# Performance work log

Hardware: AMD Instinct MI355X
Metric: run time of the kernel (lower is better)

## Reference

```python
import jax, jax.numpy as jnp
import numpy as np

# Model dims (mamba_ssm defaults: expand=2, d_state=16, d_conv=4, dt_rank=ceil(d_model/16))
V, D_MODEL, N_LAYERS = 32000, 768, 2
D_INNER, D_STATE, D_CONV, DT_RANK = 1536, 16, 4, 48
BATCH, SEQ = 2, 2048


def setup_inputs() -> dict:
    key = jax.random.key(0)
    ks = jax.random.split(key, 10)

    def nrm(k, shape, s=0.02):
        return (jax.random.normal(k, shape) * s).astype(jnp.float32)

    x = jax.random.randint(ks[0], (BATCH, SEQ), 0, V)
    emb = nrm(ks[1], (V, D_MODEL))
    # per-layer Mamba params, stacked on leading layer axis
    W_in = nrm(ks[2], (N_LAYERS, 2 * D_INNER, D_MODEL))          # in_proj (no bias)
    conv_w = nrm(ks[3], (N_LAYERS, D_INNER, 1, D_CONV), 0.1)      # depthwise causal conv
    conv_b = jnp.zeros((N_LAYERS, D_INNER), jnp.float32)
    W_x = nrm(ks[4], (N_LAYERS, DT_RANK + 2 * D_STATE, D_INNER))  # x_proj (no bias)
    W_dt = nrm(ks[5], (N_LAYERS, D_INNER, DT_RANK), 0.05)         # dt_proj
    b_dt = jnp.full((N_LAYERS, D_INNER), -4.0, jnp.float32)       # softplus(-4) ~ small dt
    # A initialized as -exp(A_log) with A_log = log(1..d_state), per mamba_ssm
    A_log = jnp.log(jnp.broadcast_to(
        jnp.arange(1, D_STATE + 1, dtype=jnp.float32), (N_LAYERS, D_INNER, D_STATE)))
    D_skip = jnp.ones((N_LAYERS, D_INNER), jnp.float32)
    W_out = nrm(ks[6], (N_LAYERS, D_MODEL, D_INNER))              # out_proj (no bias)
    ln_g = jnp.ones((D_MODEL,), jnp.float32)
    ln_b = jnp.zeros((D_MODEL,), jnp.float32)
    head_w = nrm(ks[7], (V, D_MODEL))
    head_b = jnp.zeros((V,), jnp.float32)
    return dict(x=x, emb=emb, W_in=W_in, conv_w=conv_w, conv_b=conv_b, W_x=W_x,
                W_dt=W_dt, b_dt=b_dt, A_log=A_log, D_skip=D_skip, W_out=W_out,
                ln_g=ln_g, ln_b=ln_b, head_w=head_w, head_b=head_b)


def mamba_block(h, W_in, conv_w, conv_b, W_x, W_dt, b_dt, A_log, D_skip, W_out):
    # h: (B, L, D_MODEL)
    xz = jnp.einsum('bld,ed->ble', h, W_in)              # (B, L, 2*d_inner)
    u, z = jnp.split(xz, 2, axis=-1)
    # causal depthwise conv over time
    uc = jnp.transpose(u, (0, 2, 1))                     # (B, d_inner, L)
    uc = jax.lax.conv_general_dilated(
        uc, conv_w, window_strides=(1,), padding=[(D_CONV - 1, 0)],
        feature_group_count=D_INNER, dimension_numbers=('NCH', 'OIH', 'NCH'))
    u = jax.nn.silu(jnp.transpose(uc, (0, 2, 1)) + conv_b)
    # input-dependent dt, B, C
    x_dbl = jnp.einsum('bld,ed->ble', u, W_x)            # (B, L, dt_rank+2*d_state)
    dtl, Bm, Cm = jnp.split(x_dbl, [DT_RANK, DT_RANK + D_STATE], axis=-1)
    dt = jax.nn.softplus(jnp.einsum('blr,dr->bld', dtl, W_dt) + b_dt)  # (B, L, d_inner)
    A = -jnp.exp(A_log)                                  # (d_inner, d_state)

    def step(hst, inp):
        dt_t, u_t, B_t, C_t = inp                        # (B,d_inner),(B,d_inner),(B,d_state),(B,d_state)
        hst = jnp.exp(dt_t[..., None] * A) * hst + (dt_t * u_t)[..., None] * B_t[:, None, :]
        y_t = jnp.einsum('bds,bs->bd', hst, C_t)
        return hst, y_t

    h0 = jnp.zeros((u.shape[0], D_INNER, D_STATE), u.dtype)
    xs = (dt.transpose(1, 0, 2), u.transpose(1, 0, 2),
          Bm.transpose(1, 0, 2), Cm.transpose(1, 0, 2))
    _, ys = jax.lax.scan(step, h0, xs)                   # (L, B, d_inner)
    y = ys.transpose(1, 0, 2) + u * D_skip
    y = y * jax.nn.silu(z)
    return jnp.einsum('bli,oi->blo', y, W_out)           # back to (B, L, D_MODEL)


def reference(x, emb, W_in, conv_w, conv_b, W_x, W_dt, b_dt, A_log, D_skip,
              W_out, ln_g, ln_b, head_w, head_b):
    h = emb[x]                                           # (B, L, D_MODEL)
    for l in range(N_LAYERS):
        h = h + mamba_block(h, W_in[l], conv_w[l], conv_b[l], W_x[l], W_dt[l],
                            b_dt[l], A_log[l], D_skip[l], W_out[l])
    mu = jnp.mean(h, axis=-1, keepdims=True)
    var = jnp.mean((h - mu) ** 2, axis=-1, keepdims=True)
    hn = (h - mu) * jax.lax.rsqrt(var + 1e-5) * ln_g + ln_b
    return jnp.einsum('bld,vd->blv', hn, head_w) + head_b
```

## Files before the change

kernel.cpp:

```cpp
#include <hip/hip_runtime.h>
#include <hip/hip_bf16.h>
#include <stdint.h>

#define BL    4096
#define DM    768
#define DI    1536
#define DS    16
#define DCONV 4
#define DTR   48
#define NL    2
#define SEQL  2048
#define BATCH 2
#define VOC   32000
#define NCH   32
#define CT    64

typedef __bf16 bf16_t;
typedef __bf16 bf16x8 __attribute__((ext_vector_type(8)));
typedef __bf16 bf16x4 __attribute__((ext_vector_type(4)));
typedef float  f32x4  __attribute__((ext_vector_type(4)));

__device__ __forceinline__ float sigmoidf_(float x) { return 1.f / (1.f + __expf(-x)); }

__global__ __launch_bounds__(256) void k_embed(const int* __restrict__ x,
                                               const float* __restrict__ emb,
                                               float* __restrict__ h) {
  int row = blockIdx.x;
  int tok = x[row];
  const float* e = emb + (size_t)tok * DM;
  float* hr = h + (size_t)row * DM;
  for (int c = threadIdx.x; c < DM; c += 256) hr[c] = e[c];
}

__global__ __launch_bounds__(256) void k_cvt(const float* __restrict__ src,
                                             bf16_t* __restrict__ dst, long n4) {
  long i = (long)blockIdx.x * 256 + threadIdx.x;
  if (i >= n4) return;
  float4 v = ((const float4*)src)[i];
  bf16x4 o;
  o[0] = (bf16_t)v.x; o[1] = (bf16_t)v.y; o[2] = (bf16_t)v.z; o[3] = (bf16_t)v.w;
  ((bf16x4*)dst)[i] = o;
}

__global__ __launch_bounds__(256) void k_cvt_pad(const float* __restrict__ src,
                                                 bf16_t* __restrict__ dst,
                                                 int R, int C, int srcLd, int Cpad,
                                                 long total) {
  long i = (long)blockIdx.x * 256 + threadIdx.x;
  if (i >= total) return;
  int r = (int)(i / Cpad), c = (int)(i % Cpad);
  float v = (r < R && c < C) ? src[(size_t)r * srcLd + c] : 0.f;
  dst[i] = (bf16_t)v;
}

__global__ __launch_bounds__(256) void k_conv(const float* __restrict__ xz,
                                              const float* __restrict__ cw,
                                              const float* __restrict__ cb,
                                              float* __restrict__ uc, long total) {
  long i = (long)blockIdx.x * 256 + threadIdx.x;
  if (i >= total) return;
  int d = (int)(i % DI);
  long row = i / DI;
  int l = (int)(row % SEQL);
  const float* w = cw + (size_t)d * DCONV;
  float s = cb[d];
#pragma unroll
  for (int j = 0; j < DCONV; j++) {
    int lj = l - (DCONV - 1) + j;
    if (lj >= 0) s += xz[(row - (DCONV - 1) + j) * (2 * DI) + d] * w[j];
  }
  uc[i] = s * sigmoidf_(s);
}

__global__ __launch_bounds__(256) void k_scan1(const float* __restrict__ dt,
                                               const float* __restrict__ uc,
                                               const float* __restrict__ xdbl,
                                               const float* __restrict__ A_log,
                                               float* __restrict__ cA,
                                               float* __restrict__ cB) {
  int gi = blockIdx.x * 256 + threadIdx.x;
  int s = gi & 15;
  int rest = gi >> 4;
  int d = rest % DI;
  int rest2 = rest / DI;
  int c = rest2 % NCH;
  int b = rest2 / NCH;
  float a = -__expf(A_log[d * DS + s]);
  long l0 = (long)c * CT;
  const float* dtp = dt + ((long)b * SEQL + l0) * DI + d;
  const float* ucp = uc + ((long)b * SEQL + l0) * DI + d;
  const float* Bp  = xdbl + ((long)b * SEQL + l0) * 80 + DTR + s;
  float S = 0.f, hh = 0.f;
#pragma unroll 4
  for (int l = 0; l < CT; l++) {
    float dtv = dtp[(long)l * DI];
    float uv  = ucp[(long)l * DI];
    float Bv  = Bp[(long)l * 80];
    S += dtv;
    hh = __expf(dtv * a) * hh + (dtv * uv) * Bv;
  }
  cA[gi] = __expf(a * S);
  cB[gi] = hh;
}

__global__ __launch_bounds__(256) void k_scan2(const float* __restrict__ cA,
                                               const float* __restrict__ cB,
                                               float* __restrict__ hst) {
  int gj = blockIdx.x * 256 + threadIdx.x;
  int ds_ = gj & (DI * DS - 1);
  int b = gj / (DI * DS);
  float h = 0.f;
#pragma unroll
  for (int c = 0; c < NCH; c++) {
    long idx = ((long)(b * NCH + c) * DI * DS) + ds_;
    hst[idx] = h;
    h = cA[idx] * h + cB[idx];
  }
}

__global__ __launch_bounds__(256) void k_scan3(const float* __restrict__ dt,
                                               const float* __restrict__ uc,
                                               const float* __restrict__ xdbl,
                                               const float* __restrict__ A_log,
                                               const float* __restrict__ hst,
                                               float* __restrict__ ys) {
  int gi = blockIdx.x * 256 + threadIdx.x;
  int s = gi & 15;
  int rest = gi >> 4;
  int d = rest % DI;
  int rest2 = rest / DI;
  int c = rest2 % NCH;
  int b = rest2 / NCH;
  float a = -__expf(A_log[d * DS + s]);
  long l0 = (long)c * CT;
  const float* dtp = dt + ((long)b * SEQL + l0) * DI + d;
  const float* ucp = uc + ((long)b * SEQL + l0) * DI + d;
  const float* Bp  = xdbl + ((long)b * SEQL + l0) * 80 + DTR + s;
  const float* Cp  = Bp + DS;
  float* yp = ys + ((long)b * SEQL + l0) * DI + d;
  float h = hst[gi];
#pragma unroll 4
  for (int l = 0; l < CT; l++) {
    float dtv = dtp[(long)l * DI];
    float uv  = ucp[(long)l * DI];
    float Bv  = Bp[(long)l * 80];
    float Cv  = Cp[(long)l * 80];
    h = __expf(dtv * a) * h + (dtv * uv) * Bv;
    float y = h * Cv;
    y += __shfl_xor(y, 1);
    y += __shfl_xor(y, 2);
    y += __shfl_xor(y, 4);
    y += __shfl_xor(y, 8);
    if (s == 0) yp[(long)l * DI] = y;
  }
}

__global__ __launch_bounds__(256) void k_gate(const float* __restrict__ ys,
                                              const float* __restrict__ uc,
                                              const float* __restrict__ xz,
                                              const float* __restrict__ Dsk,
                                              bf16_t* __restrict__ o, long total) {
  long i = (long)blockIdx.x * 256 + threadIdx.x;
  if (i >= total) return;
  int d = (int)(i % DI);
  long row = i / DI;
  float y = ys[i] + uc[i] * Dsk[d];
  float z = xz[row * (2 * DI) + DI + d];
  o[i] = (bf16_t)(y * z * sigmoidf_(z));
}

__global__ __launch_bounds__(256) void k_ln(const float* __restrict__ h,
                                            const float* __restrict__ g,
                                            const float* __restrict__ bta,
                                            bf16_t* __restrict__ o) {
  __shared__ float sm[4];
  int row = blockIdx.x;
  int t = threadIdx.x;
  const float* hr = h + (long)row * DM;
  float v0 = hr[t], v1 = hr[t + 256], v2 = hr[t + 512];
  float s = v0 + v1 + v2;
#pragma unroll
  for (int off = 32; off > 0; off >>= 1) s += __shfl_down(s, off);
  if ((t & 63) == 0) sm[t >> 6] = s;
  __syncthreads();
  float mu = (sm[0] + sm[1] + sm[2] + sm[3]) * (1.f / DM);
  __syncthreads();
  float d0 = v0 - mu, d1 = v1 - mu, d2 = v2 - mu;
  float q = d0 * d0 + d1 * d1 + d2 * d2;
#pragma unroll
  for (int off = 32; off > 0; off >>= 1) q += __shfl_down(q, off);
  if ((t & 63) == 0) sm[t >> 6] = q;
  __syncthreads();
  float var = (sm[0] + sm[1] + sm[2] + sm[3]) * (1.f / DM);
  float rs = rsqrtf(var + 1e-5f);
  bf16_t* orow = o + (long)row * DM;
  orow[t]       = (bf16_t)(d0 * rs * g[t]       + bta[t]);
  orow[t + 256] = (bf16_t)(d1 * rs * g[t + 256] + bta[t + 256]);
  orow[t + 512] = (bf16_t)(d2 * rs * g[t + 512] + bta[t + 512]);
}

__device__ __forceinline__ void stage16(const bf16_t* gp, bf16_t* lp) {
  __builtin_amdgcn_global_load_lds(
      (const __attribute__((address_space(1))) uint32_t*)gp,
      (__attribute__((address_space(3))) uint32_t*)lp, 16, 0, 0);
}

template <int EPI>
__global__ __launch_bounds__(256) void k_gemm(const bf16_t* __restrict__ A,
                                              const bf16_t* __restrict__ W,
                                              float* __restrict__ C,
                                              const float* __restrict__ bias,
                                              int M, int N, int K, int ldc) {
  __shared__ bf16_t lA[128 * 32];
  __shared__ bf16_t lB[128 * 32];
  const int tid = threadIdx.x;
  const int lane = tid & 63;
  const int wv = tid >> 6;
  const int wm = wv >> 1, wn = wv & 1;
  const long m0 = (long)blockIdx.y * 128;
  const long n0 = (long)blockIdx.x * 128;
  const int r0 = tid >> 2;
  const int c8 = (tid & 3) * 8;
  const int fr = lane & 15;
  const int kq = lane >> 4;

  f32x4 acc[4][4];
#pragma unroll
  for (int i = 0; i < 4; i++)
#pragma unroll
    for (int j = 0; j < 4; j++) acc[i][j] = (f32x4){0.f, 0.f, 0.f, 0.f};

  const bf16_t* Ab = A + (m0 + r0) * (long)K + c8;
  const bf16_t* Wb = W + (n0 + r0) * (long)K + c8;
  bf16_t* lAp = lA + r0 * 32 + c8;
  bf16_t* lBp = lB + r0 * 32 + c8;
  const long s64K = 64L * K;

  for (int k0 = 0; k0 < K; k0 += 32) {
    __syncthreads();
    stage16(Ab + k0, lAp);
    stage16(Ab + k0 + s64K, lAp + 64 * 32);
    stage16(Wb + k0, lBp);
    stage16(Wb + k0 + s64K, lBp + 64 * 32);
    __syncthreads();
    bf16x8 af[4], bfv[4];
#pragma unroll
    for (int f = 0; f < 4; f++)
      af[f] = *(const bf16x8*)&lA[(wm * 64 + f * 16 + fr) * 32 + kq * 8];
#pragma unroll
    for (int f = 0; f < 4; f++)
      bfv[f] = *(const bf16x8*)&lB[(wn * 64 + f * 16 + fr) * 32 + kq * 8];
#pragma unroll
    for (int fm = 0; fm < 4; fm++)
#pragma unroll
      for (int fn = 0; fn < 4; fn++)
        acc[fm][fn] = __builtin_amdgcn_mfma_f32_16x16x32_bf16(af[fm], bfv[fn],
                                                              acc[fm][fn], 0, 0, 0);
  }

  const int r4 = (lane >> 4) * 4;
  const int cc = lane & 15;
#pragma unroll
  for (int fm = 0; fm < 4; fm++) {
    long rowb = m0 + wm * 64 + fm * 16 + r4;
#pragma unroll
    for (int fn = 0; fn < 4; fn++) {
      long col = n0 + wn * 64 + fn * 16 + cc;
      if (col < N) {
        float bv = (EPI == 1 || EPI == 3) ? bias[col] : 0.f;
#pragma unroll
        for (int r = 0; r < 4; r++) {
          long row = rowb + r;
          float v = acc[fm][fn][r];
          if (EPI == 1) v += bv;
          else if (EPI == 3) { v += bv; v = (v > 20.f) ? v : log1pf(__expf(v)); }
          else if (EPI == 2) v += C[row * (long)ldc + col];
          C[row * (long)ldc + col] = v;
        }
      }
    }
  }
}


#define GLD256(ab, j, ktt, pp) do {                                             \
    int idx_ = (j) * 512 + tid;                                                 \
    int r_ = idx_ >> 3; int c16_ = idx_ & 7;                                    \
    size_t col_ = (size_t)(ktt) * 64 + (size_t)((c16_ ^ (r_ & 7)) << 3);        \
    const bf16_t* gp_ = (ab) ? (Wp + ((size_t)(n0 + r_)) * K + col_)            \
                             : (Ap + ((size_t)(m0 + r_)) * K + col_);           \
    bf16_t* lp_ = lds + ((((pp) * 2 + (ab)) * 256 + r_) * 64) + c16_ * 8;       \
    __builtin_amdgcn_global_load_lds(                                           \
        (const __attribute__((address_space(1))) uint32_t*)gp_,                 \
        (__attribute__((address_space(3))) uint32_t*)lp_, 16, 0, 0);            \
  } while (0)

#define STAGE2(pp, ktt, s) do {                                                 \
    if ((s) == 0) { GLD256(0, 0, ktt, pp); GLD256(0, 2, ktt, pp); }             \
    if ((s) == 1) { GLD256(1, 0, ktt, pp); GLD256(1, 1, ktt, pp); }             \
    if ((s) == 2) { GLD256(1, 2, ktt, pp); GLD256(1, 3, ktt, pp); }             \
    if ((s) == 3) { GLD256(0, 1, ktt, pp); GLD256(0, 3, ktt, pp); }             \
  } while (0)

#define COMPUTE256(pp, mg, kh) do {                                             \
    const char* lb_ = (const char*)lds;                                         \
    bf16x8 af_[4], bv_[4];                                                      \
    _Pragma("unroll") for (int f = 0; f < 4; ++f) {                             \
      int row_ = wm * 128 + (mg) * 64 + f * 16 + fr;                            \
      int byte_ = (((pp) * 2 + 0) * 256 + row_) * 128 +                         \
                  (((kh) * 64 + kq * 16) ^ ((row_ & 7) << 4));                  \
      af_[f] = *(const bf16x8*)(lb_ + byte_);                                   \
    }                                                                           \
    _Pragma("unroll") for (int f = 0; f < 4; ++f) {                             \
      int row_ = wn * 64 + f * 16 + fr;                                         \
      int byte_ = (((pp) * 2 + 1) * 256 + row_) * 128 +                         \
                  (((kh) * 64 + kq * 16) ^ ((row_ & 7) << 4));                  \
      bv_[f] = *(const bf16x8*)(lb_ + byte_);                                   \
    }                                                                           \
    __builtin_amdgcn_s_setprio(1);                                              \
    _Pragma("unroll") for (int fm = 0; fm < 4; ++fm)                            \
      _Pragma("unroll") for (int fn = 0; fn < 4; ++fn)                          \
        acc[(mg) * 4 + fm][fn] = __builtin_amdgcn_mfma_f32_16x16x32_bf16(       \
            af_[fm], bv_[fn], acc[(mg) * 4 + fm][fn], 0, 0, 0);                 \
    __builtin_amdgcn_s_setprio(0);                                              \
  } while (0)

#define WAITV2()  asm volatile("s_waitcnt vmcnt(2)" ::: "memory")
#define WAITV0()  asm volatile("s_waitcnt vmcnt(0)" ::: "memory")
#define BARRIER() do { __builtin_amdgcn_s_barrier();                            \
                       asm volatile("" ::: "memory"); } while (0)

template <int EPI>
__global__ __launch_bounds__(512, 2) void k_gemm256(const bf16_t* __restrict__ Ap,
                                                    const bf16_t* __restrict__ Wp,
                                                    float* __restrict__ C,
                                                    const float* __restrict__ bias,
                                                    int K, int ldc, int nxtile) {
  __shared__ bf16_t lds[2 * 2 * 256 * 64];
  const int tid = threadIdx.x;
  const int lane = tid & 63;
  const int wid = tid >> 6;
  const int wm = wid >> 2, wn = wid & 3;
  const int fr = lane & 15, kq = lane >> 4;

  const int cpx = gridDim.x >> 3;
  const int wg = ((int)blockIdx.x & 7) * cpx + ((int)blockIdx.x >> 3);
  const long m0 = (long)(wg / nxtile) * 256;
  const long n0 = (long)(wg % nxtile) * 256;

  f32x4 acc[8][4];
#pragma unroll
  for (int i = 0; i < 8; i++)
#pragma unroll
    for (int j = 0; j < 4; j++) acc[i][j] = (f32x4){0.f, 0.f, 0.f, 0.f};

  STAGE2(0, 0, 0); STAGE2(0, 0, 1); STAGE2(0, 0, 2); STAGE2(0, 0, 3);
  WAITV2();
  BARRIER();

  const int NT = K >> 6;
  for (int kt = 0; kt < NT; ++kt) {
    const int p = kt & 1;
    const bool pre = (kt + 1 < NT);
    if (pre) STAGE2(p ^ 1, kt + 1, 0);
    COMPUTE256(p, 0, 0);
    if (pre) WAITV2(); else WAITV0();
    BARRIER();
    if (pre) STAGE2(p ^ 1, kt + 1, 1);
    COMPUTE256(p, 1, 0);
    if (pre) STAGE2(p ^ 1, kt + 1, 2);
    COMPUTE256(p, 0, 1);
    if (pre) STAGE2(p ^ 1, kt + 1, 3);
    COMPUTE256(p, 1, 1);
    if (pre) {
      WAITV2();
      BARRIER();
    }
  }

  const int r4 = (lane >> 4) * 4;
  const int cc = lane & 15;
#pragma unroll
  for (int m = 0; m < 8; m++) {
    long rowb = m0 + wm * 128 + (m >> 2) * 64 + (m & 3) * 16 + r4;
#pragma unroll
    for (int n = 0; n < 4; n++) {
      long col = n0 + wn * 64 + n * 16 + cc;
      float bv = (EPI == 1) ? bias[col] : 0.f;
#pragma unroll
      for (int r = 0; r < 4; r++) {
        float v = acc[m][n][r];
        if (EPI == 1) v += bv;
        C[(rowb + r) * (long)ldc + col] = v;
      }
    }
  }
}

static inline int cdiv_l(long a, long b) { return (int)((a + b - 1) / b); }

extern "C" void kernel_launch(void* const* d_in, const int* in_sizes, int n_in,
                              void* d_out, int out_size, void* d_ws, size_t ws_size,
                              hipStream_t stream) {
  (void)in_sizes; (void)n_in; (void)out_size; (void)ws_size;
  const int*   x      = (const int*)  d_in[0];
  const float* emb    = (const float*)d_in[1];
  const float* W_in   = (const float*)d_in[2];
  const float* conv_w = (const float*)d_in[3];
  const float* conv_b = (const float*)d_in[4];
  const float* W_x    = (const float*)d_in[5];
  const float* W_dt   = (const float*)d_in[6];
  const float* b_dt   = (const float*)d_in[7];
  const float* A_log  = (const float*)d_in[8];
  const float* D_skip = (const float*)d_in[9];
  const float* W_out  = (const float*)d_in[10];
  const float* ln_g   = (const float*)d_in[11];
  const float* ln_b   = (const float*)d_in[12];
  const float* head_w = (const float*)d_in[13];
  const float* head_b = (const float*)d_in[14];
  float* out = (float*)d_out;

  char* ws = (char*)d_ws;
  bf16_t* abuf = (bf16_t*)ws;
  bf16_t* wbuf = (bf16_t*)(ws + (size_t)BL * DI * 2);

  float* xz   = out;
  float* uc   = xz   + (size_t)BL * 2 * DI;
  float* xdbl = uc   + (size_t)BL * DI;
  float* dtb  = xdbl + (size_t)BL * 80;
  float* ysb  = dtb  + (size_t)BL * DI;
  float* h    = ysb  + (size_t)BL * DI;
  float* cA   = h    + (size_t)BL * DM;
  float* cB   = cA   + (size_t)BATCH * NCH * DI * DS;
  float* hst  = cB   + (size_t)BATCH * NCH * DI * DS;

  const int scan_blocks = BATCH * NCH * DI * DS / 256;
  const int st_blocks   = BATCH * DI * DS / 256;

  k_embed<<<BL, 256, 0, stream>>>(x, emb, h);

  for (int l = 0; l < NL; ++l) {
    k_cvt<<<cdiv_l((long)BL * DM / 4, 256), 256, 0, stream>>>(h, abuf, (long)BL * DM / 4);
    k_cvt<<<cdiv_l((long)2 * DI * DM / 4, 256), 256, 0, stream>>>(
        W_in + (size_t)l * 2 * DI * DM, wbuf, (long)2 * DI * DM / 4);
    k_gemm256<0><<<(BL / 256) * (2 * DI / 256), 512, 0, stream>>>(
        abuf, wbuf, xz, nullptr, DM, 2 * DI, 2 * DI / 256);
    k_conv<<<cdiv_l((long)BL * DI, 256), 256, 0, stream>>>(
        xz, conv_w + (size_t)l * DI * DCONV, conv_b + (size_t)l * DI, uc, (long)BL * DI);
    k_cvt<<<cdiv_l((long)BL * DI / 4, 256), 256, 0, stream>>>(uc, abuf, (long)BL * DI / 4);
    k_cvt_pad<<<cdiv_l(128L * DI, 256), 256, 0, stream>>>(
        W_x + (size_t)l * 80 * DI, wbuf, 80, DI, DI, DI, 128L * DI);
    k_gemm<0><<<dim3(1, BL / 128), 256, 0, stream>>>(
        abuf, wbuf, xdbl, nullptr, BL, 80, DI, 80);
    k_cvt_pad<<<cdiv_l((long)BL * 64, 256), 256, 0, stream>>>(
        xdbl, abuf, BL, DTR, 80, 64, (long)BL * 64);
    k_cvt_pad<<<cdiv_l((long)DI * 64, 256), 256, 0, stream>>>(
        W_dt + (size_t)l * DI * DTR, wbuf, DI, DTR, DTR, 64, (long)DI * 64);
    k_gemm<3><<<dim3(DI / 128, BL / 128), 256, 0, stream>>>(
        abuf, wbuf, dtb, b_dt + (size_t)l * DI, BL, DI, 64, DI);
    k_scan1<<<scan_blocks, 256, 0, stream>>>(dtb, uc, xdbl,
                                             A_log + (size_t)l * DI * DS, cA, cB);
    k_scan2<<<st_blocks, 256, 0, stream>>>(cA, cB, hst);
    k_scan3<<<scan_blocks, 256, 0, stream>>>(dtb, uc, xdbl,
                                             A_log + (size_t)l * DI * DS, hst, ysb);
    k_gate<<<cdiv_l((long)BL * DI, 256), 256, 0, stream>>>(
        ysb, uc, xz, D_skip + (size_t)l * DI, abuf, (long)BL * DI);
    k_cvt<<<cdiv_l((long)DM * DI / 4, 256), 256, 0, stream>>>(
        W_out + (size_t)l * DM * DI, wbuf, (long)DM * DI / 4);
    k_gemm<2><<<dim3(DM / 128, BL / 128), 256, 0, stream>>>(
        abuf, wbuf, h, nullptr, BL, DM, DI, DM);
  }

  k_ln<<<BL, 256, 0, stream>>>(h, ln_g, ln_b, abuf);
  k_cvt<<<cdiv_l((long)VOC * DM / 4, 256), 256, 0, stream>>>(head_w, wbuf, (long)VOC * DM / 4);
  k_gemm256<1><<<(BL / 256) * (VOC / 256), 512, 0, stream>>>(
      abuf, wbuf, out, head_b, DM, VOC, VOC / 256);
}
```

Measured before the change: 1.016 ms.

## Fuse bf16 conversions into producer epilogues and gating into scan kernel

Producers now write bf16 copies directly: the embedding, the conv kernel, the x_proj GEMM epilogue (dt slice padded to 64) and the out_proj residual epilogue. This removes the separate conversion kernels for h, uc and the dt slice. The gate kernel is folded into scan3, so the fp32 ys buffer is never written or reread. The logits GEMM uses nontemporal stores and a hardcoded tile mapping, which saves launches and memory traffic but assumes the 16-row-tile layout.

```diff
diff --git a/kernel.cpp b/kernel.cpp
--- a/kernel.cpp
+++ b/kernel.cpp
@@ -24,12 +24,18 @@
 
 __global__ __launch_bounds__(256) void k_embed(const int* __restrict__ x,
                                                const float* __restrict__ emb,
-                                               float* __restrict__ h) {
+                                               float* __restrict__ h,
+                                               bf16_t* __restrict__ hb) {
   int row = blockIdx.x;
   int tok = x[row];
   const float* e = emb + (size_t)tok * DM;
   float* hr = h + (size_t)row * DM;
-  for (int c = threadIdx.x; c < DM; c += 256) hr[c] = e[c];
+  bf16_t* hbr = hb + (size_t)row * DM;
+  for (int c = threadIdx.x; c < DM; c += 256) {
+    float v = e[c];
+    hr[c] = v;
+    hbr[c] = (bf16_t)v;
+  }
 }
 
 __global__ __launch_bounds__(256) void k_cvt(const float* __restrict__ src,
@@ -56,7 +62,8 @@
 __global__ __launch_bounds__(256) void k_conv(const float* __restrict__ xz,
                                               const float* __restrict__ cw,
                                               const float* __restrict__ cb,
-                                              float* __restrict__ uc, long total) {
+                                              float* __restrict__ uc,
+                                              bf16_t* __restrict__ ucb, long total) {
   long i = (long)blockIdx.x * 256 + threadIdx.x;
   if (i >= total) return;
   int d = (int)(i % DI);
@@ -69,7 +76,9 @@
     int lj = l - (DCONV - 1) + j;
     if (lj >= 0) s += xz[(row - (DCONV - 1) + j) * (2 * DI) + d] * w[j];
   }
-  uc[i] = s * sigmoidf_(s);
+  float v = s * sigmoidf_(s);
+  uc[i] = v;
+  ucb[i] = (bf16_t)v;
 }
 
 __global__ __launch_bounds__(256) void k_scan1(const float* __restrict__ dt,
@@ -118,12 +127,14 @@
   }
 }
 
-__global__ __launch_bounds__(256) void k_scan3(const float* __restrict__ dt,
-                                               const float* __restrict__ uc,
-                                               const float* __restrict__ xdbl,
-                                               const float* __restrict__ A_log,
-                                               const float* __restrict__ hst,
-                                               float* __restrict__ ys) {
+__global__ __launch_bounds__(256) void k_scan3g(const float* __restrict__ dt,
+                                                const float* __restrict__ uc,
+                                                const float* __restrict__ xdbl,
+                                                const float* __restrict__ A_log,
+                                                const float* __restrict__ hst,
+                                                const float* __restrict__ xz,
+                                                const float* __restrict__ Dsk,
+                                                bf16_t* __restrict__ o) {
   int gi = blockIdx.x * 256 + threadIdx.x;
   int s = gi & 15;
   int rest = gi >> 4;
@@ -132,12 +143,14 @@
   int c = rest2 % NCH;
   int b = rest2 / NCH;
   float a = -__expf(A_log[d * DS + s]);
+  float dval = Dsk[d];
   long l0 = (long)c * CT;
   const float* dtp = dt + ((long)b * SEQL + l0) * DI + d;
   const float* ucp = uc + ((long)b * SEQL + l0) * DI + d;
   const float* Bp  = xdbl + ((long)b * SEQL + l0) * 80 + DTR + s;
   const float* Cp  = Bp + DS;
-  float* yp = ys + ((long)b * SEQL + l0) * DI + d;
+  const float* zp  = xz + ((long)b * SEQL + l0) * (2 * DI) + DI + d;
+  bf16_t* yp = o + ((long)b * SEQL + l0) * DI + d;
   float h = hst[gi];
 #pragma unroll 4
   for (int l = 0; l < CT; l++) {
@@ -151,22 +164,12 @@
     y += __shfl_xor(y, 2);
     y += __shfl_xor(y, 4);
     y += __shfl_xor(y, 8);
-    if (s == 0) yp[(long)l * DI] = y;
-  }
-}
-
-__global__ __launch_bounds__(256) void k_gate(const float* __restrict__ ys,
-                                              const float* __restrict__ uc,
-                                              const float* __restrict__ xz,
-                                              const float* __restrict__ Dsk,
-                                              bf16_t* __restrict__ o, long total) {
-  long i = (long)blockIdx.x * 256 + threadIdx.x;
-  if (i >= total) return;
-  int d = (int)(i % DI);
-  long row = i / DI;
-  float y = ys[i] + uc[i] * Dsk[d];
-  float z = xz[row * (2 * DI) + DI + d];
-  o[i] = (bf16_t)(y * z * sigmoidf_(z));
+    if (s == 0) {
+      float z = zp[(long)l * 2 * DI];
+      float yy = (y + uv * dval) * z * sigmoidf_(z);
+      yp[(long)l * DI] = (bf16_t)yy;
+    }
+  }
 }
 
 __global__ __launch_bounds__(256) void k_ln(const float* __restrict__ h,
@@ -210,6 +213,7 @@
                                               const bf16_t* __restrict__ W,
                                               float* __restrict__ C,
                                               const float* __restrict__ bias,
+                                              bf16_t* __restrict__ side,
                                               int M, int N, int K, int ldc) {
   __shared__ bf16_t lA[128 * 32];
   __shared__ bf16_t lB[128 * 32];
@@ -267,15 +271,18 @@
     for (int fn = 0; fn < 4; fn++) {
       long col = n0 + wn * 64 + fn * 16 + cc;
       if (col < N) {
-        float bv = (EPI == 1 || EPI == 3) ? bias[col] : 0.f;
+        float bv = (EPI == 3) ? bias[col] : 0.f;
 #pragma unroll
         for (int r = 0; r < 4; r++) {
           long row = rowb + r;
           float v = acc[fm][fn][r];
-          if (EPI == 1) v += bv;
-          else if (EPI == 3) { v += bv; v = (v > 20.f) ? v : log1pf(__expf(v)); }
-          else if (EPI == 2) v += C[row * (long)ldc + col];
+          if (EPI == 3) { v += bv; v = (v > 20.f) ? v : log1pf(__expf(v)); }
+          else if (EPI == 5) v += C[row * (long)ldc + col];
           C[row * (long)ldc + col] = v;
+          if (EPI == 4 && col < 64)
+            side[row * 64 + col] = (bf16_t)(col < DTR ? v : 0.f);
+          if (EPI == 5)
+            side[row * (long)ldc + col] = (bf16_t)v;
         }
       }
     }
@@ -335,7 +342,7 @@
                                                     const bf16_t* __restrict__ Wp,
                                                     float* __restrict__ C,
                                                     const float* __restrict__ bias,
-                                                    int K, int ldc, int nxtile) {
+                                                    int K, int ldc) {
   __shared__ bf16_t lds[2 * 2 * 256 * 64];
   const int tid = threadIdx.x;
   const int lane = tid & 63;
@@ -345,8 +352,8 @@
 
   const int cpx = gridDim.x >> 3;
   const int wg = ((int)blockIdx.x & 7) * cpx + ((int)blockIdx.x >> 3);
-  const long m0 = (long)(wg / nxtile) * 256;
-  const long n0 = (long)(wg % nxtile) * 256;
+  const long m0 = (long)(wg & 15) * 256;
+  const long n0 = (long)(wg >> 4) * 256;
 
   f32x4 acc[8][4];
 #pragma unroll
@@ -390,8 +397,12 @@
 #pragma unroll
       for (int r = 0; r < 4; r++) {
         float v = acc[m][n][r];
-        if (EPI == 1) v += bv;
-        C[(rowb + r) * (long)ldc + col] = v;
+        if (EPI == 1) {
+          v += bv;
+          __builtin_nontemporal_store(v, &C[(rowb + r) * (long)ldc + col]);
+        } else {
+          C[(rowb + r) * (long)ldc + col] = v;
+        }
       }
     }
   }
@@ -428,51 +439,49 @@
   float* uc   = xz   + (size_t)BL * 2 * DI;
   float* xdbl = uc   + (size_t)BL * DI;
   float* dtb  = xdbl + (size_t)BL * 80;
-  float* ysb  = dtb  + (size_t)BL * DI;
-  float* h    = ysb  + (size_t)BL * DI;
+  float* ysb_unused = dtb + (size_t)BL * DI;  (void)ysb_unused;
+  float* h    = dtb  + (size_t)BL * DI;
   float* cA   = h    + (size_t)BL * DM;
   float* cB   = cA   + (size_t)BATCH * NCH * DI * DS;
   float* hst  = cB   + (size_t)BATCH * NCH * DI * DS;
+  bf16_t* hbf = (bf16_t*)(hst + (size_t)BATCH * DI * DS);
+  bf16_t* dtl = hbf + (size_t)BL * DM;
 
   const int scan_blocks = BATCH * NCH * DI * DS / 256;
   const int st_blocks   = BATCH * DI * DS / 256;
 
-  k_embed<<<BL, 256, 0, stream>>>(x, emb, h);
+  k_embed<<<BL, 256, 0, stream>>>(x, emb, h, hbf);
 
   for (int l = 0; l < NL; ++l) {
-    k_cvt<<<cdiv_l((long)BL * DM / 4, 256), 256, 0, stream>>>(h, abuf, (long)BL * DM / 4);
     k_cvt<<<cdiv_l((long)2 * DI * DM / 4, 256), 256, 0, stream>>>(
         W_in + (size_t)l * 2 * DI * DM, wbuf, (long)2 * DI * DM / 4);
     k_gemm256<0><<<(BL / 256) * (2 * DI / 256), 512, 0, stream>>>(
-        abuf, wbuf, xz, nullptr, DM, 2 * DI, 2 * DI / 256);
+        hbf, wbuf, xz, nullptr, DM, 2 * DI);
     k_conv<<<cdiv_l((long)BL * DI, 256), 256, 0, stream>>>(
-        xz, conv_w + (size_t)l * DI * DCONV, conv_b + (size_t)l * DI, uc, (long)BL * DI);
-    k_cvt<<<cdiv_l((long)BL * DI / 4, 256), 256, 0, stream>>>(uc, abuf, (long)BL * DI / 4);
+        xz, conv_w + (size_t)l * DI * DCONV, conv_b + (size_t)l * DI,
+        uc, abuf, (long)BL * DI);
     k_cvt_pad<<<cdiv_l(128L * DI, 256), 256, 0, stream>>>(
         W_x + (size_t)l * 80 * DI, wbuf, 80, DI, DI, DI, 128L * DI);
-    k_gemm<0><<<dim3(1, BL / 128), 256, 0, stream>>>(
-        abuf, wbuf, xdbl, nullptr, BL, 80, DI, 80);
-    k_cvt_pad<<<cdiv_l((long)BL * 64, 256), 256, 0, stream>>>(
-        xdbl, abuf, BL, DTR, 80, 64, (long)BL * 64);
+    k_gemm<4><<<dim3(1, BL / 128), 256, 0, stream>>>(
+        abuf, wbuf, xdbl, nullptr, dtl, BL, 80, DI, 80);
     k_cvt_pad<<<cdiv_l((long)DI * 64, 256), 256, 0, stream>>>(
         W_dt + (size_t)l * DI * DTR, wbuf, DI, DTR, DTR, 64, (long)DI * 64);
     k_gemm<3><<<dim3(DI / 128, BL / 128), 256, 0, stream>>>(
-        abuf, wbuf, dtb, b_dt + (size_t)l * DI, BL, DI, 64, DI);
+        dtl, wbuf, dtb, b_dt + (size_t)l * DI, nullptr, BL, DI, 64, DI);
     k_scan1<<<scan_blocks, 256, 0, stream>>>(dtb, uc, xdbl,
                                              A_log + (size_t)l * DI * DS, cA, cB);
     k_scan2<<<st_blocks, 256, 0, stream>>>(cA, cB, hst);
-    k_scan3<<<scan_blocks, 256, 0, stream>>>(dtb, uc, xdbl,
-                                             A_log + (size_t)l * DI * DS, hst, ysb);
-    k_gate<<<cdiv_l((long)BL * DI, 256), 256, 0, stream>>>(
-        ysb, uc, xz, D_skip + (size_t)l * DI, abuf, (long)BL * DI);
+    k_scan3g<<<scan_blocks, 256, 0, stream>>>(dtb, uc, xdbl,
+                                              A_log + (size_t)l * DI * DS, hst,
+                                              xz, D_skip + (size_t)l * DI, abuf);
     k_cvt<<<cdiv_l((long)DM * DI / 4, 256), 256, 0, stream>>>(
         W_out + (size_t)l * DM * DI, wbuf, (long)DM * DI / 4);
-    k_gemm<2><<<dim3(DM / 128, BL / 128), 256, 0, stream>>>(
-        abuf, wbuf, h, nullptr, BL, DM, DI, DM);
+    k_gemm<5><<<dim3(DM / 128, BL / 128), 256, 0, stream>>>(
+        abuf, wbuf, h, nullptr, hbf, BL, DM, DI, DM);
   }
 
   k_ln<<<BL, 256, 0, stream>>>(h, ln_g, ln_b, abuf);
   k_cvt<<<cdiv_l((long)VOC * DM / 4, 256), 256, 0, stream>>>(head_w, wbuf, (long)VOC * DM / 4);
   k_gemm256<1><<<(BL / 256) * (VOC / 256), 512, 0, stream>>>(
-      abuf, wbuf, out, head_b, DM, VOC, VOC / 256);
-}
+      abuf, wbuf, out, head_b, DM, VOC);
+}
```

Measured after the change: 1.110 ms. +9.2%, slower.
